# Performance work log

Measured on AMD Instinct MI355X. Metric: run time of the kernel, lower is better.

## Reference

```python
import jax, jax.numpy as jnp
import numpy as np

NEG_INF = -1.0e9


def setup_inputs() -> dict:
    key = jax.random.key(0)
    k1, k2, k3, k4 = jax.random.split(key, 4)
    B, N, F, U, H = 4, 2048, 128, 64, 4
    x = jax.random.normal(k1, (B, N, F), dtype=jnp.float32)
    adj = jax.random.randint(k2, (B, N, N), 0, 2, dtype=jnp.int32)
    W = jax.random.normal(k3, (H, F, U), dtype=jnp.float32) * (1.0 / np.sqrt(F))
    b = jnp.zeros((H, U), dtype=jnp.float32)
    a_w = jax.random.normal(k4, (H, U), dtype=jnp.float32) * (1.0 / np.sqrt(U))
    a_b = jnp.zeros((H,), dtype=jnp.float32)
    return {"x": x, "adj": adj, "W": W, "b": b, "a_w": a_w, "a_b": a_b}


def reference(x, adj, W, b, a_w, a_b):
    # Per-head Dense + relu, batched over heads: proj [H,B,N,U]
    proj = jax.nn.relu(jnp.einsum('bnf,hfu->hbnu', x, W) + b[:, None, None, :])
    # Scalar attention score per node: s [H,B,N]
    s = jnp.einsum('hbnu,hu->hbn', proj, a_w) + a_b[:, None, None]
    # Outer-product logits [H,B,N,N], masked by adjacency
    logits = s[:, :, :, None] * s[:, :, None, :]
    logits = jnp.where(adj[None] > 0, logits, NEG_INF)
    scores = jax.nn.softmax(logits, axis=-1)
    # Weighted aggregation, then mean over heads -> [B,N,U]
    out = jnp.einsum('hbij,hbju->hbiu', scores, proj)
    return jnp.mean(out, axis=0)
```

## Files before the change

### kernel.cpp

```cpp
#include <hip/hip_runtime.h>
#include <hip/hip_bf16.h>


#define Bdim 4
#define Ndim 2048
#define Fdim 128
#define Udim 64
#define Hdim 4
#define JC 2
#define JCHUNK (Ndim / JC)
#define JSUB 64

typedef __attribute__((ext_vector_type(8))) short short8;
typedef __attribute__((ext_vector_type(4))) float f32x4;

__device__ __forceinline__ short bf16_rne(float f) {
  union { __hip_bfloat16 b; unsigned short u; } c;
  c.b = __float2bfloat16(f);
  return (short)c.u;
}

__device__ __forceinline__ void splitbf(float f, short& hi, short& lo) {
  unsigned u = __float_as_uint(f);
  hi = (short)(u >> 16);
  float lof = f - __uint_as_float(u & 0xffff0000u);
  lo = bf16_rne(lof);
}

__device__ __forceinline__ void stage16(const void* g, void* l) {
  __builtin_amdgcn_global_load_lds(
      (const __attribute__((address_space(1))) unsigned int*)g,
      (__attribute__((address_space(3))) unsigned int*)l, 16, 0, 0);
}

__global__ __launch_bounds__(256) void pack_adj_kernel(
    const int* __restrict__ adj, unsigned long long* __restrict__ bits,
    int nchunks) {
  const int lane = threadIdx.x & 63;
  const int wid = (blockIdx.x * 256 + threadIdx.x) >> 6;
  const int nw = (gridDim.x * 256) >> 6;
  for (int c = wid * 4; c + 3 < nchunks; c += nw * 4) {
    int v0 = adj[(size_t)(c + 0) * 64 + lane];
    int v1 = adj[(size_t)(c + 1) * 64 + lane];
    int v2 = adj[(size_t)(c + 2) * 64 + lane];
    int v3 = adj[(size_t)(c + 3) * 64 + lane];
    unsigned long long m0 = __ballot(v0 != 0);
    unsigned long long m1 = __ballot(v1 != 0);
    unsigned long long m2 = __ballot(v2 != 0);
    unsigned long long m3 = __ballot(v3 != 0);
    if (lane == 0) {
      bits[c + 0] = m0;
      bits[c + 1] = m1;
      bits[c + 2] = m2;
      bits[c + 3] = m3;
    }
  }
}

__global__ __launch_bounds__(256) void proj_kernel(
    const float* __restrict__ x, const float* __restrict__ W,
    const float* __restrict__ bias, const float* __restrict__ a_w,
    const float* __restrict__ a_b, unsigned short* __restrict__ pTh,
    unsigned short* __restrict__ pTl, float* __restrict__ s) {
  const int bid = blockIdx.x;
  const int nt = bid & 31;
  const int b = (bid >> 5) & 3;
  const int h = bid >> 7;
  const int n0 = nt * 64;

  __shared__ __align__(16) char smem[71168];
  float (*Wl)[Udim] = (float(*)[Udim])(smem);
  float (*xl)[Fdim + 4] = (float(*)[Fdim + 4])(smem + 32768);
  float (*pt)[68] = (float(*)[68])(smem + 32768);
  float* bl = (float*)(smem + 66560);
  float* awl = (float*)(smem + 66816);
  float (*sred)[16] = (float(*)[16])(smem + 67072);

  const int t = threadIdx.x;

  const float* Wg = W + (size_t)h * Fdim * Udim;
  for (int k = t; k < Fdim * Udim / 4; k += 256) {
    ((float4*)&Wl[0][0])[k] = ((const float4*)Wg)[k];
  }
  if (t < Udim) {
    bl[t] = bias[h * Udim + t];
    awl[t] = a_w[h * Udim + t];
  }
  const float* xg = x + ((size_t)b * Ndim + n0) * Fdim;
  for (int k = t; k < 64 * Fdim / 4; k += 256) {
    int row = k >> 5;
    int c4 = k & 31;
    float4 v = ((const float4*)xg)[(size_t)row * (Fdim / 4) + c4];
    *(float4*)&xl[row][c4 * 4] = v;
  }
  __syncthreads();

  const int ug = t & 15, rg = t >> 4;
  const int u0 = ug * 4, r0 = rg * 4;
  float acc[4][4] = {};

#pragma unroll 4
  for (int f = 0; f < Fdim; ++f) {
    const float4 wv = *(const float4*)&Wl[f][u0];
    const float xv[4] = {xl[r0][f], xl[r0 + 1][f], xl[r0 + 2][f], xl[r0 + 3][f]};
#pragma unroll
    for (int c = 0; c < 4; ++c) {
      acc[c][0] = fmaf(xv[c], wv.x, acc[c][0]);
      acc[c][1] = fmaf(xv[c], wv.y, acc[c][1]);
      acc[c][2] = fmaf(xv[c], wv.z, acc[c][2]);
      acc[c][3] = fmaf(xv[c], wv.w, acc[c][3]);
    }
  }

  float po[4][4];
#pragma unroll
  for (int c = 0; c < 4; ++c)
#pragma unroll
    for (int k = 0; k < 4; ++k)
      po[c][k] = fmaxf(acc[c][k] + bl[u0 + k], 0.f);

#pragma unroll
  for (int c = 0; c < 4; ++c) {
    float sp = po[c][0] * awl[u0 + 0] + po[c][1] * awl[u0 + 1] +
               po[c][2] * awl[u0 + 2] + po[c][3] * awl[u0 + 3];
    sred[r0 + c][ug] = sp;
  }
  __syncthreads();

#pragma unroll
  for (int k = 0; k < 4; ++k) {
    float4 v = {po[0][k], po[1][k], po[2][k], po[3][k]};
    *(float4*)&pt[u0 + k][r0] = v;
  }
  __syncthreads();

  const size_t hb = (size_t)h * Bdim + b;
  const int su = t >> 2;
  const int snl = (t & 3) * 16;
  float v[16];
#pragma unroll
  for (int j = 0; j < 4; ++j)
    *(float4*)&v[4 * j] = *(const float4*)&pt[su][snl + 4 * j];
  short hi[16], lo[16];
#pragma unroll
  for (int k = 0; k < 16; ++k) splitbf(v[k], hi[k], lo[k]);
  unsigned short* ph =
      pTh + hb * (size_t)(Udim * Ndim) + (size_t)su * Ndim + n0 + snl;
  unsigned short* pl =
      pTl + hb * (size_t)(Udim * Ndim) + (size_t)su * Ndim + n0 + snl;
  *(short8*)(ph + 0) = *(short8*)&hi[0];
  *(short8*)(ph + 8) = *(short8*)&hi[8];
  *(short8*)(pl + 0) = *(short8*)&lo[0];
  *(short8*)(pl + 8) = *(short8*)&lo[8];

  if (t < 64) {
    float sum = a_b[h];
#pragma unroll
    for (int k = 0; k < 16; ++k) sum += sred[t][k];
    s[hb * Ndim + n0 + t] = sum;
  }
}

__global__ __launch_bounds__(256, 3) void attn_mfma_kernel(
    const unsigned short* __restrict__ pTh,
    const unsigned short* __restrict__ pTl, const float* __restrict__ s,
    const unsigned int* __restrict__ abits, float* __restrict__ out_part,
    float* __restrict__ Z_part) {
  const int bid = blockIdx.x;
  const int jc = bid & 1;
  const int it = (bid >> 1) & 31;
  const int b = (bid >> 6) & 3;
  const int h = bid >> 8;
  const int i0g = it * 64;
  const int j0g = jc * JCHUNK;

  __shared__ float sj[JCHUNK];
  __shared__ unsigned int ab[64][33];
  __shared__ __align__(16) short Bst[2][8][1024];

  const int t = threadIdx.x;
  const int wv = t >> 6;
  const int lane = t & 63;
  const int q = lane >> 4;
  const int li = lane & 15;
  const size_t hb = (size_t)h * Bdim + b;
  const float* sg = s + hb * Ndim;

  ((float4*)sj)[t] = ((const float4*)(sg + j0g))[t];
  for (int k = t; k < 64 * 32; k += 256) {
    int row = k >> 5, w = k & 31;
    ab[row][w] =
        abits[((size_t)b * Ndim + i0g + row) * (Ndim / 32) + (j0g >> 5) + w];
  }
  const int irow = wv * 16 + li;

  const unsigned short* bsrc_h =
      pTh + hb * (size_t)(Udim * Ndim) + (size_t)(wv * 16 + li) * Ndim + j0g +
      q * 8;
  const unsigned short* bsrc_l =
      pTl + hb * (size_t)(Udim * Ndim) + (size_t)(wv * 16 + li) * Ndim + j0g +
      q * 8;

  stage16(bsrc_h + 0, &Bst[0][wv * 2 + 0][0]);
  stage16(bsrc_h + 32, &Bst[0][wv * 2 + 0][512]);
  stage16(bsrc_l + 0, &Bst[0][wv * 2 + 1][0]);
  stage16(bsrc_l + 32, &Bst[0][wv * 2 + 1][512]);

  f32x4 acc[4] = {};
  float zacc = 0.f;
  __syncthreads();

  const float si = sg[i0g + irow];
  int buf = 0;

  for (int js = 0; js < JCHUNK; js += JSUB) {
    if (js + JSUB < JCHUNK) {
      stage16(bsrc_h + js + 64, &Bst[buf ^ 1][wv * 2 + 0][0]);
      stage16(bsrc_h + js + 96, &Bst[buf ^ 1][wv * 2 + 0][512]);
      stage16(bsrc_l + js + 64, &Bst[buf ^ 1][wv * 2 + 1][0]);
      stage16(bsrc_l + js + 96, &Bst[buf ^ 1][wv * 2 + 1][512]);
    }
    const unsigned int w0 = ab[irow][(js >> 5) + 0];
    const unsigned int w1 = ab[irow][(js >> 5) + 1];
#pragma unroll
    for (int g = 0; g < 2; ++g) {
      const unsigned int mb = ((g ? w1 : w0) >> (q * 8)) & 0xffu;
      const f32x4 s0 = *(const f32x4*)&sj[js + g * 32 + q * 8];
      const f32x4 s1 = *(const f32x4*)&sj[js + g * 32 + q * 8 + 4];
      const float sv[8] = {s0.x, s0.y, s0.z, s0.w, s1.x, s1.y, s1.z, s1.w};
      short8 ahi, alo;
#pragma unroll
      for (int e = 0; e < 8; ++e) {
        float we = __expf(si * sv[e]);
        we = ((mb >> e) & 1u) ? we : 0.f;
        zacc += we;
        short hh, ll;
        splitbf(we, hh, ll);
        ahi[e] = hh;
        alo[e] = ll;
      }
      const short8 b0h = *(const short8*)&Bst[buf][0][g * 512 + lane * 8];
      const short8 b0l = *(const short8*)&Bst[buf][1][g * 512 + lane * 8];
      const short8 b1h = *(const short8*)&Bst[buf][2][g * 512 + lane * 8];
      const short8 b1l = *(const short8*)&Bst[buf][3][g * 512 + lane * 8];
      const short8 b2h = *(const short8*)&Bst[buf][4][g * 512 + lane * 8];
      const short8 b2l = *(const short8*)&Bst[buf][5][g * 512 + lane * 8];
      const short8 b3h = *(const short8*)&Bst[buf][6][g * 512 + lane * 8];
      const short8 b3l = *(const short8*)&Bst[buf][7][g * 512 + lane * 8];
      __builtin_amdgcn_s_setprio(1);
      acc[0] = __builtin_amdgcn_mfma_f32_16x16x32_bf16(ahi, b0h, acc[0], 0, 0, 0);
      acc[1] = __builtin_amdgcn_mfma_f32_16x16x32_bf16(ahi, b1h, acc[1], 0, 0, 0);
      acc[2] = __builtin_amdgcn_mfma_f32_16x16x32_bf16(ahi, b2h, acc[2], 0, 0, 0);
      acc[3] = __builtin_amdgcn_mfma_f32_16x16x32_bf16(ahi, b3h, acc[3], 0, 0, 0);
      acc[0] = __builtin_amdgcn_mfma_f32_16x16x32_bf16(alo, b0h, acc[0], 0, 0, 0);
      acc[1] = __builtin_amdgcn_mfma_f32_16x16x32_bf16(alo, b1h, acc[1], 0, 0, 0);
      acc[2] = __builtin_amdgcn_mfma_f32_16x16x32_bf16(alo, b2h, acc[2], 0, 0, 0);
      acc[3] = __builtin_amdgcn_mfma_f32_16x16x32_bf16(alo, b3h, acc[3], 0, 0, 0);
      acc[0] = __builtin_amdgcn_mfma_f32_16x16x32_bf16(ahi, b0l, acc[0], 0, 0, 0);
      acc[1] = __builtin_amdgcn_mfma_f32_16x16x32_bf16(ahi, b1l, acc[1], 0, 0, 0);
      acc[2] = __builtin_amdgcn_mfma_f32_16x16x32_bf16(ahi, b2l, acc[2], 0, 0, 0);
      acc[3] = __builtin_amdgcn_mfma_f32_16x16x32_bf16(ahi, b3l, acc[3], 0, 0, 0);
      __builtin_amdgcn_s_setprio(0);
    }
    __syncthreads();
    buf ^= 1;
  }

  zacc += __shfl_xor(zacc, 16, 64);
  zacc += __shfl_xor(zacc, 32, 64);
  const size_t pslab = ((size_t)h * JC + jc) * Bdim + b;
  if (q == 0) Z_part[pslab * Ndim + i0g + wv * 16 + li] = zacc;

  float* op = out_part + (pslab * Ndim + i0g + wv * 16) * Udim;
#pragma unroll
  for (int r = 0; r < 4; ++r) {
    const int ir = q * 4 + r;
#pragma unroll
    for (int m = 0; m < 4; ++m) {
      op[(size_t)ir * Udim + m * 16 + li] = acc[m][r];
    }
  }
}

__global__ __launch_bounds__(256) void combine_kernel(
    const float* __restrict__ out_part, const float* __restrict__ Z_part,
    float* __restrict__ out) {
  const int idx = blockIdx.x * 256 + threadIdx.x;
  const int u4 = idx & 15;
  const size_t bn = (size_t)(idx >> 4);
  float4 r = {0.f, 0.f, 0.f, 0.f};
#pragma unroll
  for (int h = 0; h < Hdim; ++h) {
    float4 p = {0.f, 0.f, 0.f, 0.f};
    float z = 0.f;
#pragma unroll
    for (int j = 0; j < JC; ++j) {
      const size_t sl = ((size_t)h * JC + j) * (Bdim * Ndim) + bn;
      float4 pj = ((const float4*)out_part)[sl * (Udim / 4) + u4];
      p.x += pj.x; p.y += pj.y; p.z += pj.z; p.w += pj.w;
      z += Z_part[sl];
    }
    z = (z != 0.f) ? z : 1.f;
    const float inv = 1.f / z;
    r.x += p.x * inv;
    r.y += p.y * inv;
    r.z += p.z * inv;
    r.w += p.w * inv;
  }
  r.x *= 0.25f; r.y *= 0.25f; r.z *= 0.25f; r.w *= 0.25f;
  ((float4*)out)[idx] = r;
}

extern "C" void kernel_launch(void* const* d_in, const int* in_sizes, int n_in,
                              void* d_out, int out_size, void* d_ws,
                              size_t ws_size, hipStream_t stream) {
  const float* x = (const float*)d_in[0];
  const int* adj = (const int*)d_in[1];
  const float* W = (const float*)d_in[2];
  const float* bias = (const float*)d_in[3];
  const float* a_w = (const float*)d_in[4];
  const float* a_b = (const float*)d_in[5];
  float* out = (float*)d_out;

  char* ws = (char*)d_ws;
  unsigned short* pTh = (unsigned short*)(ws + 0);
  unsigned short* pTl = (unsigned short*)(ws + 4194304);
  float* s = (float*)(ws + 8388608);
  unsigned int* adjbits = (unsigned int*)(ws + 8519680);
  float* out_part = (float*)(ws + 10616832);
  float* Z_part = (float*)(ws + 27394048);

  const int nchunks = Bdim * Ndim * Ndim / 64;
  pack_adj_kernel<<<2048, 256, 0, stream>>>(adj, (unsigned long long*)adjbits,
                                            nchunks);
  proj_kernel<<<Hdim * Bdim * 32, 256, 0, stream>>>(x, W, bias, a_w, a_b, pTh,
                                                    pTl, s);
  attn_mfma_kernel<<<Hdim * Bdim * 32 * JC, 256, 0, stream>>>(
      pTh, pTl, s, adjbits, out_part, Z_part);
  combine_kernel<<<(Bdim * Ndim * Udim / 4) / 256, 256, 0, stream>>>(
      out_part, Z_part, out);
}
```

Baseline: 173.1 us.

## Load B operands directly from global into registers, dropping LDS staging

Removes the LDS double buffer filled by global_load_lds and the per-iteration __syncthreads. Each wave now reads its B fragments (hi/lo projection slices) straight from global memory into two register buffers, ping-ponging them to prefetch the next 32-column step. This cuts LDS traffic and barriers but raises VGPR pressure (16 short8 buffers) and has all four waves redundantly fetch the same B data through the caches.

```diff
diff --git a/kernel.cpp b/kernel.cpp
--- a/kernel.cpp
+++ b/kernel.cpp
@@ -9,7 +9,6 @@
 #define Hdim 4
 #define JC 2
 #define JCHUNK (Ndim / JC)
-#define JSUB 64
 
 typedef __attribute__((ext_vector_type(8))) short short8;
 typedef __attribute__((ext_vector_type(4))) float f32x4;
@@ -25,12 +24,6 @@
   hi = (short)(u >> 16);
   float lof = f - __uint_as_float(u & 0xffff0000u);
   lo = bf16_rne(lof);
-}
-
-__device__ __forceinline__ void stage16(const void* g, void* l) {
-  __builtin_amdgcn_global_load_lds(
-      (const __attribute__((address_space(1))) unsigned int*)g,
-      (__attribute__((address_space(3))) unsigned int*)l, 16, 0, 0);
 }
 
 __global__ __launch_bounds__(256) void pack_adj_kernel(
@@ -161,6 +154,50 @@
   }
 }
 
+#define LOADB(dst, JS)                                       \
+  do {                                                       \
+    dst[0] = *(const short8*)(bhp + 0 * 16 * Ndim + (JS));   \
+    dst[1] = *(const short8*)(blp + 0 * 16 * Ndim + (JS));   \
+    dst[2] = *(const short8*)(bhp + 1 * 16 * Ndim + (JS));   \
+    dst[3] = *(const short8*)(blp + 1 * 16 * Ndim + (JS));   \
+    dst[4] = *(const short8*)(bhp + 2 * 16 * Ndim + (JS));   \
+    dst[5] = *(const short8*)(blp + 2 * 16 * Ndim + (JS));   \
+    dst[6] = *(const short8*)(bhp + 3 * 16 * Ndim + (JS));   \
+    dst[7] = *(const short8*)(blp + 3 * 16 * Ndim + (JS));   \
+  } while (0)
+
+#define STEP(buf, JS)                                                          \
+  do {                                                                         \
+    const unsigned int mb = (ab[irow][(JS) >> 5] >> (q * 8)) & 0xffu;          \
+    const f32x4 s0 = *(const f32x4*)&sj[(JS) + q * 8];                         \
+    const f32x4 s1 = *(const f32x4*)&sj[(JS) + q * 8 + 4];                     \
+    const float sv[8] = {s0.x, s0.y, s0.z, s0.w, s1.x, s1.y, s1.z, s1.w};      \
+    short8 ahi, alo;                                                           \
+    _Pragma("unroll") for (int e = 0; e < 8; ++e) {                            \
+      float we = __expf(si * sv[e]);                                           \
+      we = ((mb >> e) & 1u) ? we : 0.f;                                        \
+      zacc += we;                                                              \
+      short hh, ll;                                                            \
+      splitbf(we, hh, ll);                                                     \
+      ahi[e] = hh;                                                             \
+      alo[e] = ll;                                                             \
+    }                                                                          \
+    __builtin_amdgcn_s_setprio(1);                                             \
+    acc[0] = __builtin_amdgcn_mfma_f32_16x16x32_bf16(ahi, buf[0], acc[0],0,0,0);\
+    acc[1] = __builtin_amdgcn_mfma_f32_16x16x32_bf16(ahi, buf[2], acc[1],0,0,0);\
+    acc[2] = __builtin_amdgcn_mfma_f32_16x16x32_bf16(ahi, buf[4], acc[2],0,0,0);\
+    acc[3] = __builtin_amdgcn_mfma_f32_16x16x32_bf16(ahi, buf[6], acc[3],0,0,0);\
+    acc[0] = __builtin_amdgcn_mfma_f32_16x16x32_bf16(alo, buf[0], acc[0],0,0,0);\
+    acc[1] = __builtin_amdgcn_mfma_f32_16x16x32_bf16(alo, buf[2], acc[1],0,0,0);\
+    acc[2] = __builtin_amdgcn_mfma_f32_16x16x32_bf16(alo, buf[4], acc[2],0,0,0);\
+    acc[3] = __builtin_amdgcn_mfma_f32_16x16x32_bf16(alo, buf[6], acc[3],0,0,0);\
+    acc[0] = __builtin_amdgcn_mfma_f32_16x16x32_bf16(ahi, buf[1], acc[0],0,0,0);\
+    acc[1] = __builtin_amdgcn_mfma_f32_16x16x32_bf16(ahi, buf[3], acc[1],0,0,0);\
+    acc[2] = __builtin_amdgcn_mfma_f32_16x16x32_bf16(ahi, buf[5], acc[2],0,0,0);\
+    acc[3] = __builtin_amdgcn_mfma_f32_16x16x32_bf16(ahi, buf[7], acc[3],0,0,0);\
+    __builtin_amdgcn_s_setprio(0);                                             \
+  } while (0)
+
 __global__ __launch_bounds__(256, 3) void attn_mfma_kernel(
     const unsigned short* __restrict__ pTh,
     const unsigned short* __restrict__ pTl, const float* __restrict__ s,
@@ -176,7 +213,6 @@
 
   __shared__ float sj[JCHUNK];
   __shared__ unsigned int ab[64][33];
-  __shared__ __align__(16) short Bst[2][8][1024];
 
   const int t = threadIdx.x;
   const int wv = t >> 6;
@@ -194,76 +230,24 @@
   }
   const int irow = wv * 16 + li;
 
-  const unsigned short* bsrc_h =
-      pTh + hb * (size_t)(Udim * Ndim) + (size_t)(wv * 16 + li) * Ndim + j0g +
-      q * 8;
-  const unsigned short* bsrc_l =
-      pTl + hb * (size_t)(Udim * Ndim) + (size_t)(wv * 16 + li) * Ndim + j0g +
-      q * 8;
-
-  stage16(bsrc_h + 0, &Bst[0][wv * 2 + 0][0]);
-  stage16(bsrc_h + 32, &Bst[0][wv * 2 + 0][512]);
-  stage16(bsrc_l + 0, &Bst[0][wv * 2 + 1][0]);
-  stage16(bsrc_l + 32, &Bst[0][wv * 2 + 1][512]);
+  const unsigned short* bhp =
+      pTh + hb * (size_t)(Udim * Ndim) + (size_t)li * Ndim + j0g + q * 8;
+  const unsigned short* blp =
+      pTl + hb * (size_t)(Udim * Ndim) + (size_t)li * Ndim + j0g + q * 8;
 
   f32x4 acc[4] = {};
   float zacc = 0.f;
+  short8 bufA[8], bufB[8];
+  LOADB(bufA, 0);
   __syncthreads();
 
   const float si = sg[i0g + irow];
-  int buf = 0;
-
-  for (int js = 0; js < JCHUNK; js += JSUB) {
-    if (js + JSUB < JCHUNK) {
-      stage16(bsrc_h + js + 64, &Bst[buf ^ 1][wv * 2 + 0][0]);
-      stage16(bsrc_h + js + 96, &Bst[buf ^ 1][wv * 2 + 0][512]);
-      stage16(bsrc_l + js + 64, &Bst[buf ^ 1][wv * 2 + 1][0]);
-      stage16(bsrc_l + js + 96, &Bst[buf ^ 1][wv * 2 + 1][512]);
-    }
-    const unsigned int w0 = ab[irow][(js >> 5) + 0];
-    const unsigned int w1 = ab[irow][(js >> 5) + 1];
-#pragma unroll
-    for (int g = 0; g < 2; ++g) {
-      const unsigned int mb = ((g ? w1 : w0) >> (q * 8)) & 0xffu;
-      const f32x4 s0 = *(const f32x4*)&sj[js + g * 32 + q * 8];
-      const f32x4 s1 = *(const f32x4*)&sj[js + g * 32 + q * 8 + 4];
-      const float sv[8] = {s0.x, s0.y, s0.z, s0.w, s1.x, s1.y, s1.z, s1.w};
-      short8 ahi, alo;
-#pragma unroll
-      for (int e = 0; e < 8; ++e) {
-        float we = __expf(si * sv[e]);
-        we = ((mb >> e) & 1u) ? we : 0.f;
-        zacc += we;
-        short hh, ll;
-        splitbf(we, hh, ll);
-        ahi[e] = hh;
-        alo[e] = ll;
-      }
-      const short8 b0h = *(const short8*)&Bst[buf][0][g * 512 + lane * 8];
-      const short8 b0l = *(const short8*)&Bst[buf][1][g * 512 + lane * 8];
-      const short8 b1h = *(const short8*)&Bst[buf][2][g * 512 + lane * 8];
-      const short8 b1l = *(const short8*)&Bst[buf][3][g * 512 + lane * 8];
-      const short8 b2h = *(const short8*)&Bst[buf][4][g * 512 + lane * 8];
-      const short8 b2l = *(const short8*)&Bst[buf][5][g * 512 + lane * 8];
-      const short8 b3h = *(const short8*)&Bst[buf][6][g * 512 + lane * 8];
-      const short8 b3l = *(const short8*)&Bst[buf][7][g * 512 + lane * 8];
-      __builtin_amdgcn_s_setprio(1);
-      acc[0] = __builtin_amdgcn_mfma_f32_16x16x32_bf16(ahi, b0h, acc[0], 0, 0, 0);
-      acc[1] = __builtin_amdgcn_mfma_f32_16x16x32_bf16(ahi, b1h, acc[1], 0, 0, 0);
-      acc[2] = __builtin_amdgcn_mfma_f32_16x16x32_bf16(ahi, b2h, acc[2], 0, 0, 0);
-      acc[3] = __builtin_amdgcn_mfma_f32_16x16x32_bf16(ahi, b3h, acc[3], 0, 0, 0);
-      acc[0] = __builtin_amdgcn_mfma_f32_16x16x32_bf16(alo, b0h, acc[0], 0, 0, 0);
-      acc[1] = __builtin_amdgcn_mfma_f32_16x16x32_bf16(alo, b1h, acc[1], 0, 0, 0);
-      acc[2] = __builtin_amdgcn_mfma_f32_16x16x32_bf16(alo, b2h, acc[2], 0, 0, 0);
-      acc[3] = __builtin_amdgcn_mfma_f32_16x16x32_bf16(alo, b3h, acc[3], 0, 0, 0);
-      acc[0] = __builtin_amdgcn_mfma_f32_16x16x32_bf16(ahi, b0l, acc[0], 0, 0, 0);
-      acc[1] = __builtin_amdgcn_mfma_f32_16x16x32_bf16(ahi, b1l, acc[1], 0, 0, 0);
-      acc[2] = __builtin_amdgcn_mfma_f32_16x16x32_bf16(ahi, b2l, acc[2], 0, 0, 0);
-      acc[3] = __builtin_amdgcn_mfma_f32_16x16x32_bf16(ahi, b3l, acc[3], 0, 0, 0);
-      __builtin_amdgcn_s_setprio(0);
-    }
-    __syncthreads();
-    buf ^= 1;
+
+  for (int js = 0; js < JCHUNK; js += 64) {
+    LOADB(bufB, js + 32);
+    STEP(bufA, js);
+    if (js + 64 < JCHUNK) LOADB(bufA, js + 64);
+    STEP(bufB, js + 32);
   }
 
   zacc += __shfl_xor(zacc, 16, 64);
```

After: 239.1 us. 38.1% more time.
